# Kernel tuning notes

Measured on AMD Instinct MI355X. Metric: run time of the kernel, lower is better.

The kernel has to match this reference:

```python
import jax, jax.numpy as jnp
import numpy as np

N = 2048        # tokens (batch*seq)
H = 4096        # hidden_size (LLaMA-7B)
I = 11008       # intermediate_size (LLaMA-7B)
QMAX = 127.0    # int8 symmetric quant range


def setup_inputs() -> dict:
    key = jax.random.key(0)
    ks = jax.random.split(key, 6)
    # pre-quantized int8 activations (stored as int32) + per-token dynamic scales
    x_q = jax.random.randint(ks[0], (N, H), -127, 128, dtype=jnp.int32)
    x_scale = jax.random.uniform(ks[1], (N,), dtype=jnp.float32) * 0.01 + 1e-4
    # fused [gate; up] int8 weight [2I, H] with per-output-channel scales
    w_gateup = jax.random.randint(ks[2], (2 * I, H), -127, 128, dtype=jnp.int32)
    w_gateup_scale = jax.random.uniform(ks[3], (2 * I,), dtype=jnp.float32) * 0.005 + 1e-4
    # down_proj int8 weight [H, I] with per-output-channel scales
    w_down = jax.random.randint(ks[4], (H, I), -127, 128, dtype=jnp.int32)
    w_down_scale = jax.random.uniform(ks[5], (H,), dtype=jnp.float32) * 0.005 + 1e-4
    return {"x_q": x_q, "x_scale": x_scale, "w_gateup": w_gateup,
            "w_gateup_scale": w_gateup_scale, "w_down": w_down,
            "w_down_scale": w_down_scale}


def reference(x_q, x_scale, w_gateup, w_gateup_scale, w_down, w_down_scale):
    acc = jnp.matmul(x_q, w_gateup.T)                      # [N, 2I] int32
    gateup = acc.astype(jnp.float32) * x_scale[:, None] * w_gateup_scale[None, :]
    # --- fused silu_and_mul + dynamic per-token requantization ---
    gate, up = jnp.split(gateup, 2, axis=-1)               # each [N, I]
    act = jax.nn.silu(gate) * up                           # [N, I]
    s2 = jnp.max(jnp.abs(act), axis=-1) / QMAX             # [N] dynamic scale
    q2 = jnp.clip(jnp.round(act / s2[:, None]), -QMAX, QMAX)  # requantized int8 (as f32)
    out = jnp.matmul(q2, w_down.T.astype(jnp.float32)) * s2[:, None] * w_down_scale[None, :]
    return out                                             # [N, H]
```

## Files before the change

### kernel.cpp

```cpp
#include <hip/hip_runtime.h>
#include <stdint.h>

typedef int i32x4 __attribute__((ext_vector_type(4)));
typedef unsigned short u16x8 __attribute__((ext_vector_type(8)));

#define N_TOK 2048
#define HID   4096
#define INTER 11008
#define TWOI  22016
#define KT1   64
#define KT2   172

#define GLD16(gp, lp) __builtin_amdgcn_global_load_lds( \
    (const __attribute__((address_space(1))) void*)(gp), \
    (__attribute__((address_space(3))) void*)(lp), 16, 0, 0)
#define BAR() __builtin_amdgcn_s_barrier()
#define WVM(n) asm volatile("s_waitcnt vmcnt(" #n ")" ::: "memory")
#define LGKM0() do { asm volatile("s_waitcnt lgkmcnt(0)" ::: "memory"); \
                     __builtin_amdgcn_sched_barrier(0); } while (0)

__device__ __forceinline__ unsigned short f2bf(float f) {
  uint32_t u = __float_as_uint(f);
  uint32_t r = (u + 0x7fffu + ((u >> 16) & 1u)) >> 16;
  return (unsigned short)r;
}

__device__ __forceinline__ float bf2f(unsigned short b) {
  return __uint_as_float(((uint32_t)b) << 16);
}

__global__ __launch_bounds__(256) void pack_frag(
    const int* __restrict__ src, uint8_t* __restrict__ dst,
    int lgPR, int KT, int K)
{
  const int u = blockIdx.x * 256 + threadIdx.x;
  const int l = u & 63;
  const int rest = u >> 6;
  const int f = rest & ((1 << (lgPR - 4)) - 1);
  const int s = rest >> (lgPR - 4);
  const int p = s / KT;
  const int kt = s - p * KT;
  const int row = (p << lgPR) + f * 16 + (l & 15);
  const int col = kt * 64 + ((l >> 4) << 4);
  const int* sp = src + (size_t)row * K + col;
  i32x4 o;
#pragma unroll
  for (int qq = 0; qq < 4; ++qq) {
    i32x4 w = *reinterpret_cast<const i32x4*>(sp + qq * 4);
    o[qq] = (w[0] & 255) | ((w[1] & 255) << 8) | ((w[2] & 255) << 16)
          | ((w[3] & 255) << 24);
  }
  *reinterpret_cast<i32x4*>(dst + (size_t)u * 16) = o;
}

__global__ __launch_bounds__(256) void pack_gufrag(
    const int* __restrict__ src, uint8_t* __restrict__ dst)
{
  const int u = blockIdx.x * 256 + threadIdx.x;
  const int l = u & 63;
  const int rest = u >> 6;
  const int fi = rest & 15;
  const int s = rest >> 4;
  const int p = s / KT1;
  const int kt = s - p * KT1;
  const int base = p * 128 + ((fi >> 1) << 4) + (l & 15);
  const int srow = (fi & 1) ? (INTER + base) : base;
  const int col = kt * 64 + ((l >> 4) << 4);
  const int* sp = src + (size_t)srow * HID + col;
  i32x4 o;
#pragma unroll
  for (int qq = 0; qq < 4; ++qq) {
    i32x4 w = *reinterpret_cast<const i32x4*>(sp + qq * 4);
    o[qq] = (w[0] & 255) | ((w[1] & 255) << 8) | ((w[2] & 255) << 16)
          | ((w[3] & 255) << 24);
  }
  *reinterpret_cast<i32x4*>(dst + (size_t)u * 16) = o;
}

__global__ __launch_bounds__(1024) void zero_mx(float* __restrict__ mx) {
  const int i = blockIdx.x * 1024 + threadIdx.x;
  if (i < N_TOK) mx[i] = 0.0f;
}

__global__ __launch_bounds__(512, 2) void gemm1_k(
    const uint8_t* __restrict__ x8p, const uint8_t* __restrict__ wgp,
    const float* __restrict__ xs, const float* __restrict__ wgs,
    unsigned short* __restrict__ act, float* __restrict__ mx)
{
  __shared__ uint8_t sm[131072];
  const int tid = threadIdx.x;
  const int lane = tid & 63, wid = tid >> 6;
  const int wgm = wid >> 2, wgn = wid & 3;
  const int r15 = lane & 15;
  const int l16 = lane * 16;
  const int aBase = (wgm << 13) + l16;
  const int bBase = 16384 + (wgn << 12) + l16;

  const int bid = blockIdx.x;
  const int v = (bid & 7) * 86 + (bid >> 3);
  const int mt = v & 7;
  const int ntB = v >> 3;

  const uint8_t* pA = x8p + (size_t)mt  * (KT1 * 16384) + tid * 16;
  const uint8_t* pB = wgp + (size_t)ntB * (KT1 * 16384) + tid * 16;

  i32x4 acc[8][4] = {};

#define STG1(t, s) do {                                        \
    uint8_t* l = sm + (s) * 32768 + tid * 16;                  \
    const uint8_t* aa = pA + (size_t)(t) * 16384;              \
    GLD16(aa, l);                                              \
    GLD16(aa + 8192, l + 8192);                                \
    const uint8_t* bb = pB + (size_t)(t) * 16384;              \
    GLD16(bb, l + 16384);                                      \
    GLD16(bb + 8192, l + 24576);                               \
  } while (0)

  STG1(0, 0); STG1(1, 1); STG1(2, 2);
  WVM(8); BAR();

  for (int t = 0; t < KT1; ++t) {
    const int rem = KT1 - 1 - t;
    const uint8_t* b = sm + (t & 3) * 32768;
    uint8_t* lnx = sm + ((t + 3) & 3) * 32768 + tid * 16;
    i32x4 bv[4], av[4];
#pragma unroll
    for (int n = 0; n < 4; ++n)
      bv[n] = *reinterpret_cast<const i32x4*>(b + bBase + n * 1024);
#pragma unroll
    for (int m = 0; m < 4; ++m)
      av[m] = *reinterpret_cast<const i32x4*>(b + aBase + m * 1024);
    if (rem >= 3) {
      const uint8_t* bb = pB + (size_t)(t + 3) * 16384;
      GLD16(bb, lnx + 16384);
      GLD16(bb + 8192, lnx + 24576);
    }
    BAR();
    LGKM0();
    __builtin_amdgcn_s_setprio(1);
#pragma unroll
    for (int m = 0; m < 4; ++m)
#pragma unroll
      for (int n = 0; n < 4; ++n)
        acc[m][n] = __builtin_amdgcn_mfma_i32_16x16x64_i8(
            av[m], bv[n], acc[m][n], 0, 0, 0);
    __builtin_amdgcn_s_setprio(0);
#pragma unroll
    for (int m = 0; m < 4; ++m)
      av[m] = *reinterpret_cast<const i32x4*>(b + aBase + (m + 4) * 1024);
    if (rem >= 3) {
      const uint8_t* aa = pA + (size_t)(t + 3) * 16384;
      GLD16(aa, lnx);
      GLD16(aa + 8192, lnx + 8192);
      WVM(8);
    } else if (rem == 2) { WVM(4); }
    else if (rem == 1)   { WVM(0); }
    BAR();
    LGKM0();
    __builtin_amdgcn_s_setprio(1);
#pragma unroll
    for (int m = 0; m < 4; ++m)
#pragma unroll
      for (int n = 0; n < 4; ++n)
        acc[m + 4][n] = __builtin_amdgcn_mfma_i32_16x16x64_i8(
            av[m], bv[n], acc[m + 4][n], 0, 0, 0);
    __builtin_amdgcn_s_setprio(0);
  }
#undef STG1

  __syncthreads();
  float* smred = (float*)sm;
  const int rq = (lane >> 4) << 2;
#pragma unroll
  for (int m = 0; m < 8; ++m) {
    float am[4] = {0.f, 0.f, 0.f, 0.f};
#pragma unroll
    for (int p = 0; p < 2; ++p) {
      const int colb = ntB * 128 + (wgn << 5) + (p << 4) + r15;
      const float gsc = wgs[colb];
      const float usc = wgs[INTER + colb];
#pragma unroll
      for (int r = 0; r < 4; ++r) {
        const int rowl = (wgm << 7) + m * 16 + rq + r;
        const int grow = mt * 256 + rowl;
        const float xr = xs[grow];
        const float g  = (float)acc[m][2 * p][r] * xr * gsc;
        const float uv = (float)acc[m][2 * p + 1][r] * xr * usc;
        const float a  = g / (1.f + __expf(-g)) * uv;
        act[(size_t)grow * INTER + colb] = f2bf(a);
        am[r] = fmaxf(am[r], __builtin_fabsf(a));
      }
    }
#pragma unroll
    for (int r = 0; r < 4; ++r)
#pragma unroll
      for (int off = 1; off < 16; off <<= 1)
        am[r] = fmaxf(am[r], __shfl_xor(am[r], off, 64));
    if (r15 == 0) {
#pragma unroll
      for (int r = 0; r < 4; ++r)
        smred[wgn * 256 + (wgm << 7) + m * 16 + rq + r] = am[r];
    }
  }
  __syncthreads();
  if (tid < 256) {
    const float vmx = fmaxf(fmaxf(smred[tid], smred[256 + tid]),
                            fmaxf(smred[512 + tid], smred[768 + tid]));
    atomicMax((int*)&mx[mt * 256 + tid], __float_as_int(vmx));
  }
}

__global__ __launch_bounds__(256) void quant_k(
    const unsigned short* __restrict__ act, const float* __restrict__ mx,
    uint8_t* __restrict__ q2p)
{
  const int u = blockIdx.x * 256 + threadIdx.x;
  const int l = u & 63;
  const int rest = u >> 6;
  const int f = rest & 7;
  const int s = rest >> 3;
  const int mt = s / KT2;
  const int t = s - mt * KT2;
  const int row = mt * 128 + f * 16 + (l & 15);
  const int col = t * 64 + ((l >> 4) << 4);
  const unsigned short* ap = act + (size_t)row * INTER + col;
  const float inv = 127.0f / fmaxf(mx[row], 1e-30f);
  u16x8 a0 = *reinterpret_cast<const u16x8*>(ap);
  u16x8 a1 = *reinterpret_cast<const u16x8*>(ap + 8);
  i32x4 o;
#pragma unroll
  for (int qq = 0; qq < 4; ++qq) {
    uint32_t d = 0;
#pragma unroll
    for (int b = 0; b < 4; ++b) {
      const int j = qq * 4 + b;
      float af = bf2f((j < 8) ? a0[j] : a1[j - 8]);
      float rr = rintf(af * inv);
      rr = fminf(fmaxf(rr, -127.f), 127.f);
      d |= ((uint32_t)((int)rr & 255)) << (8 * b);
    }
    o[qq] = (int)d;
  }
  *reinterpret_cast<i32x4*>(q2p + (size_t)u * 16) = o;
}

__global__ __launch_bounds__(512, 2) void gemm2_k(
    const uint8_t* __restrict__ q2p, const uint8_t* __restrict__ wdp,
    const float* __restrict__ mx, const float* __restrict__ wds,
    float* __restrict__ out)
{
  __shared__ uint8_t sm[98304];
  const int tid = threadIdx.x;
  const int lane = tid & 63, wid = tid >> 6;
  const int wgm = wid >> 2, wgn = wid & 3;
  const int r15 = lane & 15;
  const int l16 = lane * 16;
  const int aBase = (wgm << 12) + l16;
  const int bBase = 8192 + (wgn << 12) + l16;

  const int bid = blockIdx.x;
  const int v = (bid & 7) * 32 + (bid >> 3);
  const int nt = v >> 4, mt = v & 15;

  const uint8_t* pA = q2p + (size_t)mt * (KT2 * 8192)  + tid * 16;
  const uint8_t* pB = wdp + (size_t)nt * (KT2 * 16384) + tid * 16;

  i32x4 acc[4][4] = {};

#define STG2(t, s) do {                                        \
    uint8_t* l = sm + (s) * 24576 + tid * 16;                  \
    GLD16(pA + (size_t)(t) * 8192, l);                         \
    const uint8_t* bb = pB + (size_t)(t) * 16384;              \
    GLD16(bb, l + 8192);                                       \
    GLD16(bb + 8192, l + 16384);                               \
  } while (0)

  STG2(0, 0); STG2(1, 1); STG2(2, 2);
  WVM(6); BAR();

  for (int t = 0; t < KT2; ++t) {
    const int rem = KT2 - 1 - t;
    const uint8_t* b = sm + (t & 3) * 24576;
    uint8_t* lnx = sm + ((t + 3) & 3) * 24576 + tid * 16;
    i32x4 bv[4], av[2];
#pragma unroll
    for (int n = 0; n < 4; ++n)
      bv[n] = *reinterpret_cast<const i32x4*>(b + bBase + n * 1024);
#pragma unroll
    for (int m = 0; m < 2; ++m)
      av[m] = *reinterpret_cast<const i32x4*>(b + aBase + m * 1024);
    if (rem >= 3) {
      const uint8_t* bb = pB + (size_t)(t + 3) * 16384;
      GLD16(bb, lnx + 8192);
      GLD16(bb + 8192, lnx + 16384);
    }
    BAR();
    LGKM0();
    __builtin_amdgcn_s_setprio(1);
#pragma unroll
    for (int m = 0; m < 2; ++m)
#pragma unroll
      for (int n = 0; n < 4; ++n)
        acc[m][n] = __builtin_amdgcn_mfma_i32_16x16x64_i8(
            av[m], bv[n], acc[m][n], 0, 0, 0);
    __builtin_amdgcn_s_setprio(0);
#pragma unroll
    for (int m = 0; m < 2; ++m)
      av[m] = *reinterpret_cast<const i32x4*>(b + aBase + (m + 2) * 1024);
    if (rem >= 3) {
      GLD16(pA + (size_t)(t + 3) * 8192, lnx);
      WVM(6);
    } else if (rem == 2) { WVM(3); }
    else if (rem == 1)   { WVM(0); }
    BAR();
    LGKM0();
    __builtin_amdgcn_s_setprio(1);
#pragma unroll
    for (int m = 0; m < 2; ++m)
#pragma unroll
      for (int n = 0; n < 4; ++n)
        acc[m + 2][n] = __builtin_amdgcn_mfma_i32_16x16x64_i8(
            av[m], bv[n], acc[m + 2][n], 0, 0, 0);
    __builtin_amdgcn_s_setprio(0);
  }
#undef STG2

  const int rq = (lane >> 4) << 2;
#pragma unroll
  for (int m = 0; m < 4; ++m) {
#pragma unroll
    for (int r = 0; r < 4; ++r) {
      const int rowl = (wgm << 6) + m * 16 + rq + r;
      const int grow = mt * 128 + rowl;
      const float s2 = mx[grow] * (1.0f / 127.0f);
      float* op = out + (size_t)grow * HID + nt * 256 + (wgn << 6) + r15;
      const float* wp = wds + nt * 256 + (wgn << 6) + r15;
#pragma unroll
      for (int n = 0; n < 4; ++n)
        op[n * 16] = (float)acc[m][n][r] * s2 * wp[n * 16];
    }
  }
}

extern "C" void kernel_launch(void* const* d_in, const int* in_sizes, int n_in,
                              void* d_out, int out_size, void* d_ws, size_t ws_size,
                              hipStream_t stream)
{
  const int*   x_q = (const int*)d_in[0];
  const float* xs  = (const float*)d_in[1];
  const int*   wg  = (const int*)d_in[2];
  const float* wgs = (const float*)d_in[3];
  const int*   wd  = (const int*)d_in[4];
  const float* wds = (const float*)d_in[5];
  float* out = (float*)d_out;

  uint8_t* ws = (uint8_t*)d_ws;
  uint8_t* x8p = ws;
  uint8_t* wgp = x8p + 8388608;
  uint8_t* wdp = wgp + 90177536;
  unsigned short* act = (unsigned short*)(wdp + 45088768);
  float* mx = (float*)((uint8_t*)act + 45088768);
  uint8_t* q2p = (uint8_t*)mx + 8192;

  zero_mx<<<2, 1024, 0, stream>>>(mx);
  pack_frag<<<2048, 256, 0, stream>>>(x_q, x8p, 8, KT1, HID);
  pack_gufrag<<<22016, 256, 0, stream>>>(wg, wgp);
  pack_frag<<<11008, 256, 0, stream>>>(wd, wdp, 8, KT2, INTER);

  gemm1_k<<<688, 512, 0, stream>>>(x8p, wgp, xs, wgs, act, mx);
  quant_k<<<5504, 256, 0, stream>>>(act, mx, q2p);
  gemm2_k<<<256, 512, 0, stream>>>(q2p, wdp, mx, wds, out);
}
```

Measured before the change: 424.4 us.

## Replace LDS staging with register double-buffered direct global loads in both GEMMs

Both int8 GEMM kernels drop the shared-memory ring buffer, its global_load_lds staging and the barriers. Each wave now loads its own A/B fragments straight from global memory into two register sets, alternating loads and MFMA blocks. This removes LDS traffic and barrier synchronisation. In exchange, data shared across waves in a block is fetched redundantly from global/L2, and register pressure rises substantially.

```diff
diff --git a/kernel.cpp b/kernel.cpp
--- a/kernel.cpp
+++ b/kernel.cpp
@@ -10,14 +10,6 @@
 #define TWOI  22016
 #define KT1   64
 #define KT2   172
-
-#define GLD16(gp, lp) __builtin_amdgcn_global_load_lds( \
-    (const __attribute__((address_space(1))) void*)(gp), \
-    (__attribute__((address_space(3))) void*)(lp), 16, 0, 0)
-#define BAR() __builtin_amdgcn_s_barrier()
-#define WVM(n) asm volatile("s_waitcnt vmcnt(" #n ")" ::: "memory")
-#define LGKM0() do { asm volatile("s_waitcnt lgkmcnt(0)" ::: "memory"); \
-                     __builtin_amdgcn_sched_barrier(0); } while (0)
 
 __device__ __forceinline__ unsigned short f2bf(float f) {
   uint32_t u = __float_as_uint(f);
@@ -87,89 +79,57 @@
     const float* __restrict__ xs, const float* __restrict__ wgs,
     unsigned short* __restrict__ act, float* __restrict__ mx)
 {
-  __shared__ uint8_t sm[131072];
+  __shared__ float smred[1024];
   const int tid = threadIdx.x;
   const int lane = tid & 63, wid = tid >> 6;
   const int wgm = wid >> 2, wgn = wid & 3;
   const int r15 = lane & 15;
   const int l16 = lane * 16;
-  const int aBase = (wgm << 13) + l16;
-  const int bBase = 16384 + (wgn << 12) + l16;
 
   const int bid = blockIdx.x;
   const int v = (bid & 7) * 86 + (bid >> 3);
   const int mt = v & 7;
   const int ntB = v >> 3;
 
-  const uint8_t* pA = x8p + (size_t)mt  * (KT1 * 16384) + tid * 16;
-  const uint8_t* pB = wgp + (size_t)ntB * (KT1 * 16384) + tid * 16;
+  const uint8_t* pA = x8p + (size_t)mt  * (KT1 * 16384) + (wgm << 13) + l16;
+  const uint8_t* pB = wgp + (size_t)ntB * (KT1 * 16384) + (wgn << 12) + l16;
 
   i32x4 acc[8][4] = {};
-
-#define STG1(t, s) do {                                        \
-    uint8_t* l = sm + (s) * 32768 + tid * 16;                  \
-    const uint8_t* aa = pA + (size_t)(t) * 16384;              \
-    GLD16(aa, l);                                              \
-    GLD16(aa + 8192, l + 8192);                                \
-    const uint8_t* bb = pB + (size_t)(t) * 16384;              \
-    GLD16(bb, l + 16384);                                      \
-    GLD16(bb + 8192, l + 24576);                               \
+  i32x4 aA[8], bA[4], aB[8], bB[4];
+
+#define LD1(AS, BS, t) do {                                          \
+    const uint8_t* ap_ = pA + (size_t)(t) * 16384;                   \
+    const uint8_t* bp_ = pB + (size_t)(t) * 16384;                   \
+    _Pragma("unroll")                                                \
+    for (int m = 0; m < 8; ++m)                                      \
+      AS[m] = *reinterpret_cast<const i32x4*>(ap_ + m * 1024);       \
+    _Pragma("unroll")                                                \
+    for (int n = 0; n < 4; ++n)                                      \
+      BS[n] = *reinterpret_cast<const i32x4*>(bp_ + n * 1024);       \
   } while (0)
 
-  STG1(0, 0); STG1(1, 1); STG1(2, 2);
-  WVM(8); BAR();
-
-  for (int t = 0; t < KT1; ++t) {
-    const int rem = KT1 - 1 - t;
-    const uint8_t* b = sm + (t & 3) * 32768;
-    uint8_t* lnx = sm + ((t + 3) & 3) * 32768 + tid * 16;
-    i32x4 bv[4], av[4];
-#pragma unroll
-    for (int n = 0; n < 4; ++n)
-      bv[n] = *reinterpret_cast<const i32x4*>(b + bBase + n * 1024);
-#pragma unroll
-    for (int m = 0; m < 4; ++m)
-      av[m] = *reinterpret_cast<const i32x4*>(b + aBase + m * 1024);
-    if (rem >= 3) {
-      const uint8_t* bb = pB + (size_t)(t + 3) * 16384;
-      GLD16(bb, lnx + 16384);
-      GLD16(bb + 8192, lnx + 24576);
-    }
-    BAR();
-    LGKM0();
-    __builtin_amdgcn_s_setprio(1);
-#pragma unroll
-    for (int m = 0; m < 4; ++m)
-#pragma unroll
-      for (int n = 0; n < 4; ++n)
-        acc[m][n] = __builtin_amdgcn_mfma_i32_16x16x64_i8(
-            av[m], bv[n], acc[m][n], 0, 0, 0);
-    __builtin_amdgcn_s_setprio(0);
-#pragma unroll
-    for (int m = 0; m < 4; ++m)
-      av[m] = *reinterpret_cast<const i32x4*>(b + aBase + (m + 4) * 1024);
-    if (rem >= 3) {
-      const uint8_t* aa = pA + (size_t)(t + 3) * 16384;
-      GLD16(aa, lnx);
-      GLD16(aa + 8192, lnx + 8192);
-      WVM(8);
-    } else if (rem == 2) { WVM(4); }
-    else if (rem == 1)   { WVM(0); }
-    BAR();
-    LGKM0();
-    __builtin_amdgcn_s_setprio(1);
-#pragma unroll
-    for (int m = 0; m < 4; ++m)
-#pragma unroll
-      for (int n = 0; n < 4; ++n)
-        acc[m + 4][n] = __builtin_amdgcn_mfma_i32_16x16x64_i8(
-            av[m], bv[n], acc[m + 4][n], 0, 0, 0);
-    __builtin_amdgcn_s_setprio(0);
-  }
-#undef STG1
-
-  __syncthreads();
-  float* smred = (float*)sm;
+#define MM1(AS, BS) do {                                             \
+    __builtin_amdgcn_s_setprio(1);                                   \
+    _Pragma("unroll")                                                \
+    for (int m = 0; m < 8; ++m)                                      \
+      _Pragma("unroll")                                              \
+      for (int n = 0; n < 4; ++n)                                    \
+        acc[m][n] = __builtin_amdgcn_mfma_i32_16x16x64_i8(           \
+            AS[m], BS[n], acc[m][n], 0, 0, 0);                       \
+    __builtin_amdgcn_s_setprio(0);                                   \
+  } while (0)
+
+  LD1(aA, bA, 0);
+#pragma unroll 1
+  for (int t = 0; t < KT1; t += 2) {
+    if (t + 1 < KT1) LD1(aB, bB, t + 1);
+    MM1(aA, bA);
+    if (t + 2 < KT1) LD1(aA, bA, t + 2);
+    MM1(aB, bB);
+  }
+#undef LD1
+#undef MM1
+
   const int rq = (lane >> 4) << 2;
 #pragma unroll
   for (int m = 0; m < 8; ++m) {
@@ -249,81 +209,54 @@
     const float* __restrict__ mx, const float* __restrict__ wds,
     float* __restrict__ out)
 {
-  __shared__ uint8_t sm[98304];
   const int tid = threadIdx.x;
   const int lane = tid & 63, wid = tid >> 6;
   const int wgm = wid >> 2, wgn = wid & 3;
   const int r15 = lane & 15;
   const int l16 = lane * 16;
-  const int aBase = (wgm << 12) + l16;
-  const int bBase = 8192 + (wgn << 12) + l16;
 
   const int bid = blockIdx.x;
   const int v = (bid & 7) * 32 + (bid >> 3);
   const int nt = v >> 4, mt = v & 15;
 
-  const uint8_t* pA = q2p + (size_t)mt * (KT2 * 8192)  + tid * 16;
-  const uint8_t* pB = wdp + (size_t)nt * (KT2 * 16384) + tid * 16;
+  const uint8_t* pA = q2p + (size_t)mt * (KT2 * 8192)  + (wgm << 12) + l16;
+  const uint8_t* pB = wdp + (size_t)nt * (KT2 * 16384) + (wgn << 12) + l16;
 
   i32x4 acc[4][4] = {};
-
-#define STG2(t, s) do {                                        \
-    uint8_t* l = sm + (s) * 24576 + tid * 16;                  \
-    GLD16(pA + (size_t)(t) * 8192, l);                         \
-    const uint8_t* bb = pB + (size_t)(t) * 16384;              \
-    GLD16(bb, l + 8192);                                       \
-    GLD16(bb + 8192, l + 16384);                               \
+  i32x4 aA[4], bA[4], aB[4], bB[4];
+
+#define LD2(AS, BS, t) do {                                          \
+    const uint8_t* ap_ = pA + (size_t)(t) * 8192;                    \
+    const uint8_t* bp_ = pB + (size_t)(t) * 16384;                   \
+    _Pragma("unroll")                                                \
+    for (int m = 0; m < 4; ++m)                                      \
+      AS[m] = *reinterpret_cast<const i32x4*>(ap_ + m * 1024);       \
+    _Pragma("unroll")                                                \
+    for (int n = 0; n < 4; ++n)                                      \
+      BS[n] = *reinterpret_cast<const i32x4*>(bp_ + n * 1024);       \
   } while (0)
 
-  STG2(0, 0); STG2(1, 1); STG2(2, 2);
-  WVM(6); BAR();
-
-  for (int t = 0; t < KT2; ++t) {
-    const int rem = KT2 - 1 - t;
-    const uint8_t* b = sm + (t & 3) * 24576;
-    uint8_t* lnx = sm + ((t + 3) & 3) * 24576 + tid * 16;
-    i32x4 bv[4], av[2];
-#pragma unroll
-    for (int n = 0; n < 4; ++n)
-      bv[n] = *reinterpret_cast<const i32x4*>(b + bBase + n * 1024);
-#pragma unroll
-    for (int m = 0; m < 2; ++m)
-      av[m] = *reinterpret_cast<const i32x4*>(b + aBase + m * 1024);
-    if (rem >= 3) {
-      const uint8_t* bb = pB + (size_t)(t + 3) * 16384;
-      GLD16(bb, lnx + 8192);
-      GLD16(bb + 8192, lnx + 16384);
-    }
-    BAR();
-    LGKM0();
-    __builtin_amdgcn_s_setprio(1);
-#pragma unroll
-    for (int m = 0; m < 2; ++m)
-#pragma unroll
-      for (int n = 0; n < 4; ++n)
-        acc[m][n] = __builtin_amdgcn_mfma_i32_16x16x64_i8(
-            av[m], bv[n], acc[m][n], 0, 0, 0);
-    __builtin_amdgcn_s_setprio(0);
-#pragma unroll
-    for (int m = 0; m < 2; ++m)
-      av[m] = *reinterpret_cast<const i32x4*>(b + aBase + (m + 2) * 1024);
-    if (rem >= 3) {
-      GLD16(pA + (size_t)(t + 3) * 8192, lnx);
-      WVM(6);
-    } else if (rem == 2) { WVM(3); }
-    else if (rem == 1)   { WVM(0); }
-    BAR();
-    LGKM0();
-    __builtin_amdgcn_s_setprio(1);
-#pragma unroll
-    for (int m = 0; m < 2; ++m)
-#pragma unroll
-      for (int n = 0; n < 4; ++n)
-        acc[m + 2][n] = __builtin_amdgcn_mfma_i32_16x16x64_i8(
-            av[m], bv[n], acc[m + 2][n], 0, 0, 0);
-    __builtin_amdgcn_s_setprio(0);
-  }
-#undef STG2
+#define MM2(AS, BS) do {                                             \
+    __builtin_amdgcn_s_setprio(1);                                   \
+    _Pragma("unroll")                                                \
+    for (int m = 0; m < 4; ++m)                                      \
+      _Pragma("unroll")                                              \
+      for (int n = 0; n < 4; ++n)                                    \
+        acc[m][n] = __builtin_amdgcn_mfma_i32_16x16x64_i8(           \
+            AS[m], BS[n], acc[m][n], 0, 0, 0);                       \
+    __builtin_amdgcn_s_setprio(0);                                   \
+  } while (0)
+
+  LD2(aA, bA, 0);
+#pragma unroll 1
+  for (int t = 0; t < KT2; t += 2) {
+    if (t + 1 < KT2) LD2(aB, bB, t + 1);
+    MM2(aA, bA);
+    if (t + 2 < KT2) LD2(aA, bA, t + 2);
+    MM2(aB, bB);
+  }
+#undef LD2
+#undef MM2
 
   const int rq = (lane >> 4) << 2;
 #pragma unroll
```

Result: slower. 499.3 us (+17.6%).
